# Kernel tuning notes

Hardware: AMD Instinct MI355X
Metric: run time of the kernel (lower is better)

Reference implementation:

```python
import jax, jax.numpy as jnp
import numpy as np

TOP_K = 4


def setup_inputs() -> dict:
    key = jax.random.key(0)
    ks = jax.random.split(key, 5)
    B, T, D = 2, 1024, 1024
    P, PD = 256, 32  # n_patterns, pattern_dim
    return {
        "x": jax.random.normal(ks[0], (B, T, D), dtype=jnp.float32),
        "hasher_w": jax.random.normal(ks[1], (PD, D), dtype=jnp.float32) * 0.03,
        "keys": jax.random.normal(ks[2], (P, PD), dtype=jnp.float32) * 0.1,
        "values_down": jax.random.normal(ks[3], (P, D, PD), dtype=jnp.float32) * 0.01,
        "values_up": jax.random.normal(ks[4], (P, PD, D), dtype=jnp.float32) * 0.01,
        "scale": jnp.full((1,), 0.1, dtype=jnp.float32),
    }


def reference(x, hasher_w, keys, values_down, values_up, scale):
    # h = hasher(x): [B,T,pattern_dim]
    h = jnp.einsum("btd,pd->btp", x, hasher_w)
    # similarity to pattern keys: [B,T,n_patterns]
    sim = jnp.einsum("btp,np->btn", h, keys)
    vals, idx = jax.lax.top_k(sim, TOP_K)          # [B,T,TOP_K]
    w = jax.nn.softmax(vals, axis=-1)              # softmax over the top-k scores
    out = jnp.zeros_like(x)
    for k in range(TOP_K):  # small fixed loop, matches original
        ik = idx[..., k]                            # [B,T] int32
        vd = values_down[ik]                        # [B,T,D,PD] gathered per-token
        vu = values_up[ik]                          # [B,T,PD,D]
        proj = jax.nn.silu(jnp.einsum("btd,btdp->btp", x, vd))
        o = jnp.einsum("btp,btpd->btd", proj, vu)
        out = out + o * w[..., k:k + 1]
    return x + out * scale
```

## Files before the change

### kernel.cpp

```cpp
#include <hip/hip_runtime.h>
#include <math.h>
#include <float.h>

#define DDIM 1024
#define PDIM 32
#define NPAT 256
#define TOPK 4
#define BLOCK 256
#define GT   16
#define DCHP 128
#define NCHP 8
#define RTPB 4

__global__ __launch_bounds__(BLOCK) void route_kernel(
    const float* __restrict__ x,
    const float* __restrict__ hasher_w,
    const float* __restrict__ keys,
    int*   __restrict__ tki,
    float* __restrict__ tkw,
    int*   __restrict__ gcount,
    int ntok)
{
    __shared__ float shmem[RTPB * 64 * 33];
    __shared__ float h_s[RTPB][32];

    const int tid  = threadIdx.x;
    const int wv   = tid >> 6;
    const int lane = tid & 63;
    const int traw = blockIdx.x * RTPB + wv;
    const int tok  = min(traw, ntok - 1);

    const float4* xrow = (const float4*)(x + (size_t)tok * DDIM);
    float4 xr[4];
    #pragma unroll
    for (int i = 0; i < 4; ++i) xr[i] = xrow[i * 64 + lane];

    float part[PDIM];
    #pragma unroll
    for (int pp = 0; pp < PDIM; ++pp) part[pp] = 0.f;

    float* hs = shmem;
    for (int i = 0; i < 4; ++i) {
        #pragma unroll
        for (int k = 0; k < 8; ++k) {
            const int q  = k * 256 + tid;
            const int pp = q >> 6, fi = q & 63;
            ((float4*)hs)[q] =
                *(const float4*)(hasher_w + (size_t)pp * DDIM + i * 256 + fi * 4);
        }
        __syncthreads();
        #pragma unroll
        for (int pp = 0; pp < PDIM; ++pp) {
            const float4 w4 = *(const float4*)&hs[pp * 256 + lane * 4];
            part[pp] = fmaf(xr[i].x, w4.x, part[pp]);
            part[pp] = fmaf(xr[i].y, w4.y, part[pp]);
            part[pp] = fmaf(xr[i].z, w4.z, part[pp]);
            part[pp] = fmaf(xr[i].w, w4.w, part[pp]);
        }
        __syncthreads();
    }

    float* P = shmem + wv * (64 * 33);
    #pragma unroll
    for (int pp = 0; pp < PDIM; ++pp) P[lane * 33 + pp] = part[pp];
    __syncthreads();

    {
        const int pp = lane & 31, half = lane >> 5;
        float hsum = 0.f;
        #pragma unroll 8
        for (int i = 0; i < 32; ++i)
            hsum += P[(half * 32 + i) * 33 + pp];
        hsum += __shfl_xor(hsum, 32, 64);
        if (half == 0) h_s[wv][pp] = hsum;
    }
    __syncthreads();

    float4 h4[8];
    #pragma unroll
    for (int i = 0; i < 8; ++i) h4[i] = *(const float4*)&h_s[wv][i * 4];

    float sc0, sc1, sc2, sc3;
    {
        float sv[4];
        #pragma unroll
        for (int c = 0; c < 4; ++c) {
            const float4* kr = (const float4*)(keys + (size_t)(c * 64 + lane) * PDIM);
            float a = 0.f;
            #pragma unroll
            for (int i = 0; i < 8; ++i) {
                const float4 k4 = kr[i];
                a = fmaf(k4.x, h4[i].x, a); a = fmaf(k4.y, h4[i].y, a);
                a = fmaf(k4.z, h4[i].z, a); a = fmaf(k4.w, h4[i].w, a);
            }
            sv[c] = a;
        }
        sc0 = sv[0]; sc1 = sv[1]; sc2 = sv[2]; sc3 = sv[3];
    }

    float wval[TOPK]; int widx[TOPK];
    #pragma unroll
    for (int r = 0; r < TOPK; ++r) {
        float bv = sc0; int bc = 0;
        if (sc1 > bv) { bv = sc1; bc = 1; }
        if (sc2 > bv) { bv = sc2; bc = 2; }
        if (sc3 > bv) { bv = sc3; bc = 3; }
        int bidx = bc * 64 + lane;
        #pragma unroll
        for (int off = 1; off < 64; off <<= 1) {
            const float ov = __shfl_xor(bv, off, 64);
            const int   oi = __shfl_xor(bidx, off, 64);
            if (ov > bv || (ov == bv && oi < bidx)) { bv = ov; bidx = oi; }
        }
        wval[r] = bv; widx[r] = bidx;
        if ((bidx & 63) == lane) {
            const int c = bidx >> 6;
            if (c == 0) sc0 = -FLT_MAX;
            else if (c == 1) sc1 = -FLT_MAX;
            else if (c == 2) sc2 = -FLT_MAX;
            else sc3 = -FLT_MAX;
        }
    }

    if (lane == 0 && traw < ntok) {
        float m = wval[0];
        #pragma unroll
        for (int k = 1; k < TOPK; ++k) m = fmaxf(m, wval[k]);
        float s = 0.f, e[TOPK];
        #pragma unroll
        for (int k = 0; k < TOPK; ++k) { e[k] = expf(wval[k] - m); s += e[k]; }
        #pragma unroll
        for (int k = 0; k < TOPK; ++k) {
            tki[tok * TOPK + k] = widx[k];
            tkw[tok * TOPK + k] = e[k] / s;
            atomicAdd(&gcount[widx[k]], 1);
        }
    }
}

__global__ __launch_bounds__(NPAT) void scan_kernel(
    const int* __restrict__ gcount,
    int* __restrict__ offs,
    int* __restrict__ gcur,
    int* __restrict__ tile2p, int* __restrict__ tilei,
    int maxt)
{
    __shared__ int s[NPAT];
    const int tid = threadIdx.x;

    const int v = gcount[tid];
    s[tid] = v;
    __syncthreads();
    for (int off = 1; off < NPAT; off <<= 1) {
        int t = 0;
        if (tid >= off) t = s[tid - off];
        __syncthreads();
        s[tid] += t;
        __syncthreads();
    }
    const int incl = s[tid];
    offs[tid + 1] = incl;
    if (tid == 0) offs[0] = 0;
    gcur[tid] = incl - v;

    const int tc = (v + GT - 1) / GT;
    __syncthreads();
    s[tid] = tc;
    __syncthreads();
    for (int off = 1; off < NPAT; off <<= 1) {
        int t = 0;
        if (tid >= off) t = s[tid - off];
        __syncthreads();
        s[tid] += t;
        __syncthreads();
    }
    const int toff = s[tid] - tc;
    for (int i = tid; i < maxt; i += NPAT) tile2p[i] = -1;
    __syncthreads();
    for (int i = 0; i < tc; ++i) { tile2p[toff + i] = tid; tilei[toff + i] = i; }
}

__global__ __launch_bounds__(BLOCK) void fill_kernel(
    const int* __restrict__ tki, const float* __restrict__ tkw,
    const float* __restrict__ scale_p,
    int* __restrict__ gcur,
    int* __restrict__ etok, float* __restrict__ ew, int* __restrict__ slotof,
    int nent)
{
    const int e = blockIdx.x * BLOCK + threadIdx.x;
    if (e >= nent) return;
    const int p = tki[e];
    const int slot = atomicAdd(&gcur[p], 1);
    etok[slot] = e >> 2;
    ew[slot]   = tkw[e] * scale_p[0];
    slotof[e]  = slot;
}

__global__ __launch_bounds__(BLOCK, 6) void proj_kernel(
    const float* __restrict__ x,
    const float* __restrict__ vd,
    const int* __restrict__ offs,
    const int* __restrict__ etok,
    const int* __restrict__ tile2p,
    const int* __restrict__ tilei,
    float* __restrict__ part,
    int nent)
{
    __shared__ float vd_s[DCHP * PDIM];
    __shared__ float x_s[GT * DCHP];
    __shared__ int   gt[GT];
    __shared__ int   gs[GT];

    const int tb  = blockIdx.x >> 3;
    const int c   = blockIdx.x & 7;
    const int p   = tile2p[tb];
    if (p < 0) return;
    const int tid = threadIdx.x;
    const int off0 = offs[p] + tilei[tb] * GT;
    const int gv   = min(GT, offs[p + 1] - off0);

    const float* vdp = vd + (size_t)p * DDIM * PDIM + (size_t)c * DCHP * PDIM;
    #pragma unroll
    for (int k = 0; k < 4; ++k)
        ((float4*)vd_s)[k * 256 + tid] = ((const float4*)vdp)[k * 256 + tid];

    if (tid < GT) {
        if (tid < gv) { gt[tid] = etok[off0 + tid]; gs[tid] = off0 + tid; }
        else          { gt[tid] = etok[off0];       gs[tid] = nent; }
    }
    __syncthreads();

    #pragma unroll
    for (int k = 0; k < 2; ++k) {
        const int q  = k * 256 + tid;
        const int g  = q >> 5, fi = q & 31;
        ((float4*)x_s)[g * 32 + fi] =
            *(const float4*)(x + (size_t)gt[g] * DDIM + c * DCHP + fi * 4);
    }
    __syncthreads();

    const int lane = tid & 63;
    const int wv   = tid >> 6;
    const int pp4  = lane & 7;
    const int seg  = lane >> 3;

    float4 acc[4];
    #pragma unroll
    for (int j = 0; j < 4; ++j) acc[j] = make_float4(0.f, 0.f, 0.f, 0.f);

    #pragma unroll
    for (int i4 = 0; i4 < 4; ++i4) {
        const int d0 = seg * 16 + i4 * 4;
        const float4 v0 = *(const float4*)&vd_s[(d0 + 0) * PDIM + pp4 * 4];
        const float4 v1 = *(const float4*)&vd_s[(d0 + 1) * PDIM + pp4 * 4];
        const float4 v2 = *(const float4*)&vd_s[(d0 + 2) * PDIM + pp4 * 4];
        const float4 v3 = *(const float4*)&vd_s[(d0 + 3) * PDIM + pp4 * 4];
        #pragma unroll
        for (int j = 0; j < 4; ++j) {
            const float4 xg = *(const float4*)&x_s[(wv * 4 + j) * DCHP + d0];
            acc[j].x = fmaf(xg.x, v0.x, acc[j].x);
            acc[j].y = fmaf(xg.x, v0.y, acc[j].y);
            acc[j].z = fmaf(xg.x, v0.z, acc[j].z);
            acc[j].w = fmaf(xg.x, v0.w, acc[j].w);
            acc[j].x = fmaf(xg.y, v1.x, acc[j].x);
            acc[j].y = fmaf(xg.y, v1.y, acc[j].y);
            acc[j].z = fmaf(xg.y, v1.z, acc[j].z);
            acc[j].w = fmaf(xg.y, v1.w, acc[j].w);
            acc[j].x = fmaf(xg.z, v2.x, acc[j].x);
            acc[j].y = fmaf(xg.z, v2.y, acc[j].y);
            acc[j].z = fmaf(xg.z, v2.z, acc[j].z);
            acc[j].w = fmaf(xg.z, v2.w, acc[j].w);
            acc[j].x = fmaf(xg.w, v3.x, acc[j].x);
            acc[j].y = fmaf(xg.w, v3.y, acc[j].y);
            acc[j].z = fmaf(xg.w, v3.z, acc[j].z);
            acc[j].w = fmaf(xg.w, v3.w, acc[j].w);
        }
    }

    #pragma unroll
    for (int j = 0; j < 4; ++j) {
        #pragma unroll
        for (int off = 8; off <= 32; off <<= 1) {
            acc[j].x += __shfl_xor(acc[j].x, off, 64);
            acc[j].y += __shfl_xor(acc[j].y, off, 64);
            acc[j].z += __shfl_xor(acc[j].z, off, 64);
            acc[j].w += __shfl_xor(acc[j].w, off, 64);
        }
    }

    float* partc = part + (size_t)c * (size_t)(nent + 1) * PDIM;
    if ((lane & 0x38) == 0) {
        #pragma unroll
        for (int j = 0; j < 4; ++j)
            *(float4*)&partc[(size_t)gs[wv * 4 + j] * PDIM + pp4 * 4] = acc[j];
    }
}

template <int MODE>
__global__ __launch_bounds__(BLOCK, 6) void up_kernel(
    const float* __restrict__ vu,
    const int* __restrict__ offs,
    const int* __restrict__ etok,
    const float* __restrict__ ew,
    const int* __restrict__ tile2p,
    const int* __restrict__ tilei,
    const float* __restrict__ part,
    float* __restrict__ dst,
    int nent)
{
    __shared__ float vu_s[PDIM * DCHP];
    __shared__ float projT[PDIM][20];
    __shared__ int   gt[GT];
    __shared__ float gw[GT];
    __shared__ int   gs[GT];

    const int tb  = blockIdx.x >> 3;
    const int c   = blockIdx.x & 7;
    const int p   = tile2p[tb];
    if (p < 0) return;
    const int tid = threadIdx.x;
    const int off0 = offs[p] + tilei[tb] * GT;
    const int gv   = min(GT, offs[p + 1] - off0);

    const size_t PS = (size_t)(nent + 1) * PDIM;

    const float* vup = vu + (size_t)p * PDIM * DDIM + (size_t)c * DCHP;
    #pragma unroll
    for (int k = 0; k < 4; ++k) {
        const int q  = k * 256 + tid;
        const int pp = q >> 5, fi = q & 31;
        *(float4*)&vu_s[pp * DCHP + fi * 4] =
            *(const float4*)(vup + (size_t)pp * DDIM + fi * 4);
    }
    if (tid < GT) {
        if (tid < gv) {
            gt[tid] = etok[off0 + tid];
            gw[tid] = ew[off0 + tid];
            gs[tid] = off0 + tid;
        } else {
            gt[tid] = etok[off0]; gw[tid] = 0.f; gs[tid] = nent;
        }
    }
    __syncthreads();

    #pragma unroll
    for (int r = 0; r < 2; ++r) {
        const int idx = tid + r * BLOCK;
        const int g = idx >> 5, pp = idx & 31;
        const size_t row = (size_t)gs[g] * PDIM + pp;
        float s = 0.f;
        #pragma unroll
        for (int i = 0; i < NCHP; ++i) s += part[i * PS + row];
        const float pj = s / (1.f + expf(-s));
        projT[pp][g] = pj * gw[g];
    }
    __syncthreads();

    const int tg  = tid >> 5;
    const int l32 = tid & 31;
    const int g0 = tg * 2, g1 = tg * 2 + 1;

    float4 o0 = make_float4(0.f, 0.f, 0.f, 0.f);
    float4 o1 = o0;
    #pragma unroll
    for (int pp = 0; pp < PDIM; ++pp) {
        const float4 vu4 = *(const float4*)&vu_s[pp * DCHP + l32 * 4];
        const float a = projT[pp][g0];
        const float b = projT[pp][g1];
        o0.x = fmaf(a, vu4.x, o0.x); o0.y = fmaf(a, vu4.y, o0.y);
        o0.z = fmaf(a, vu4.z, o0.z); o0.w = fmaf(a, vu4.w, o0.w);
        o1.x = fmaf(b, vu4.x, o1.x); o1.y = fmaf(b, vu4.y, o1.y);
        o1.z = fmaf(b, vu4.z, o1.z); o1.w = fmaf(b, vu4.w, o1.w);
    }

    if (MODE == 0) {
        *(float4*)(dst + (size_t)gs[g0] * DDIM + c * DCHP + l32 * 4) = o0;
        *(float4*)(dst + (size_t)gs[g1] * DDIM + c * DCHP + l32 * 4) = o1;
    } else {
        if (g0 < gv) {
            float* op = dst + (size_t)gt[g0] * DDIM + c * DCHP + l32 * 4;
            atomicAdd(op + 0, o0.x); atomicAdd(op + 1, o0.y);
            atomicAdd(op + 2, o0.z); atomicAdd(op + 3, o0.w);
        }
        if (g1 < gv) {
            float* op = dst + (size_t)gt[g1] * DDIM + c * DCHP + l32 * 4;
            atomicAdd(op + 0, o1.x); atomicAdd(op + 1, o1.y);
            atomicAdd(op + 2, o1.z); atomicAdd(op + 3, o1.w);
        }
    }
}

__global__ __launch_bounds__(BLOCK) void combine_kernel(
    const float* __restrict__ x, const float* __restrict__ contrib,
    const int* __restrict__ slotof, float* __restrict__ out)
{
    __shared__ int sl[TOPK];
    const int t = blockIdx.x, tid = threadIdx.x;
    if (tid < TOPK) sl[tid] = slotof[t * TOPK + tid];
    __syncthreads();
    float4 r = ((const float4*)(x + (size_t)t * DDIM))[tid];
    #pragma unroll
    for (int k = 0; k < TOPK; ++k) {
        const float4 cv = ((const float4*)(contrib + (size_t)sl[k] * DDIM))[tid];
        r.x += cv.x; r.y += cv.y; r.z += cv.z; r.w += cv.w;
    }
    ((float4*)(out + (size_t)t * DDIM))[tid] = r;
}

extern "C" void kernel_launch(void* const* d_in, const int* in_sizes, int n_in,
                              void* d_out, int out_size, void* d_ws, size_t ws_size,
                              hipStream_t stream) {
    const float* x        = (const float*)d_in[0];
    const float* hasher_w = (const float*)d_in[1];
    const float* keys     = (const float*)d_in[2];
    const float* vd       = (const float*)d_in[3];
    const float* vu       = (const float*)d_in[4];
    const float* scale    = (const float*)d_in[5];
    float* out = (float*)d_out;

    const int ntok = in_sizes[0] / DDIM;
    if (ntok <= 0) return;
    const int nent = ntok * TOPK;
    const int maxt = (nent + GT - 1) / GT + NPAT;

    char* w = (char*)d_ws;
    const size_t o_gcnt = 0;
    const size_t o_gcur = 1024;
    const size_t o_offs = 2048;
    const size_t o_tki  = 4096;
    const size_t o_tkw  = o_tki  + (size_t)nent * 4;
    const size_t o_etok = o_tkw  + (size_t)nent * 4;
    const size_t o_ew   = o_etok + (size_t)nent * 4;
    const size_t o_slot = o_ew   + (size_t)nent * 4;
    const size_t o_t2p  = o_slot + (size_t)nent * 4;
    const size_t o_tli  = o_t2p  + (size_t)maxt * 4;
    const size_t o_part = (o_tli + (size_t)maxt * 4 + 255) & ~(size_t)255;
    const size_t partsz = (size_t)NCHP * (size_t)(nent + 1) * PDIM * 4;
    const size_t o_ctb  = (o_part + partsz + 255) & ~(size_t)255;
    const size_t needPart    = o_ctb;
    const size_t needContrib = o_ctb + (size_t)(nent + 1) * DDIM * 4;

    int*   gcount = (int*)(w + o_gcnt);
    int*   gcur   = (int*)(w + o_gcur);
    int*   offs   = (int*)(w + o_offs);
    int*   tki    = (int*)(w + o_tki);
    float* tkw    = (float*)(w + o_tkw);
    int*   etok   = (int*)(w + o_etok);
    float* ew     = (float*)(w + o_ew);
    int*   slotof = (int*)(w + o_slot);
    int*   tile2p = (int*)(w + o_t2p);
    int*   tilei  = (int*)(w + o_tli);
    float* part   = (float*)(w + o_part);
    float* contrib= (float*)(w + o_ctb);

    hipMemsetAsync(gcount, 0, NPAT * sizeof(int), stream);

    const int rblocks = (ntok + RTPB - 1) / RTPB;
    hipLaunchKernelGGL(route_kernel, dim3(rblocks), dim3(BLOCK), 0, stream,
                       x, hasher_w, keys, tki, tkw, gcount, ntok);
    hipLaunchKernelGGL(scan_kernel, dim3(1), dim3(NPAT), 0, stream,
                       gcount, offs, gcur, tile2p, tilei, maxt);
    hipLaunchKernelGGL(fill_kernel, dim3((nent + BLOCK - 1) / BLOCK), dim3(BLOCK),
                       0, stream, tki, tkw, scale, gcur, etok, ew, slotof, nent);
    hipLaunchKernelGGL(proj_kernel, dim3(maxt * NCHP), dim3(BLOCK), 0, stream,
                       x, vd, offs, etok, tile2p, tilei, part, nent);

    if (ws_size >= needContrib) {
        hipLaunchKernelGGL((up_kernel<0>), dim3(maxt * NCHP), dim3(BLOCK), 0, stream,
                           vu, offs, etok, ew, tile2p, tilei, part, contrib, nent);
        hipLaunchKernelGGL(combine_kernel, dim3(ntok), dim3(BLOCK), 0, stream,
                           x, contrib, slotof, out);
    } else if (ws_size >= needPart) {
        hipMemcpyAsync(out, x, (size_t)ntok * DDIM * 4, hipMemcpyDeviceToDevice,
                       stream);
        hipLaunchKernelGGL((up_kernel<1>), dim3(maxt * NCHP), dim3(BLOCK), 0, stream,
                           vu, offs, etok, ew, tile2p, tilei, part, out, nent);
    }
}
```

Baseline: 186.0 us.

## Fuse down and up projections into one kernel, route two tokens per wave

The separate proj and up kernels are merged into one fused kernel per tile. It loops over all eight D-chunks, first for the down projection (accumulated in registers) and then for the up projection. This removes the partial-sum workspace round-trip and one launch. The catch is eight times fewer blocks, each running a serial chunk loop with many barriers, under launch bounds lowered to 3. The routing kernel now handles two tokens per wave, reusing each staged hasher tile for twice the FMAs.

```diff
diff --git a/kernel.cpp b/kernel.cpp
--- a/kernel.cpp
+++ b/kernel.cpp
@@ -10,7 +10,7 @@
 #define GT   16
 #define DCHP 128
 #define NCHP 8
-#define RTPB 4
+#define RTPB 8
 
 __global__ __launch_bounds__(BLOCK) void route_kernel(
     const float* __restrict__ x,
@@ -21,23 +21,28 @@
     int*   __restrict__ gcount,
     int ntok)
 {
-    __shared__ float shmem[RTPB * 64 * 33];
-    __shared__ float h_s[RTPB][32];
+    __shared__ float shmem[4 * 64 * 33];
+    __shared__ float h_s[4][2][PDIM];
 
     const int tid  = threadIdx.x;
     const int wv   = tid >> 6;
     const int lane = tid & 63;
-    const int traw = blockIdx.x * RTPB + wv;
-    const int tok  = min(traw, ntok - 1);
-
-    const float4* xrow = (const float4*)(x + (size_t)tok * DDIM);
-    float4 xr[4];
-    #pragma unroll
-    for (int i = 0; i < 4; ++i) xr[i] = xrow[i * 64 + lane];
-
-    float part[PDIM];
-    #pragma unroll
-    for (int pp = 0; pp < PDIM; ++pp) part[pp] = 0.f;
+    const int traw0 = blockIdx.x * RTPB + wv * 2;
+    const int traw1 = traw0 + 1;
+    const int tok0 = min(traw0, ntok - 1);
+    const int tok1 = min(traw1, ntok - 1);
+
+    float4 xr0[4], xr1[4];
+    {
+        const float4* p0 = (const float4*)(x + (size_t)tok0 * DDIM);
+        const float4* p1 = (const float4*)(x + (size_t)tok1 * DDIM);
+        #pragma unroll
+        for (int i = 0; i < 4; ++i) { xr0[i] = p0[i * 64 + lane]; xr1[i] = p1[i * 64 + lane]; }
+    }
+
+    float part0[PDIM], part1[PDIM];
+    #pragma unroll
+    for (int pp = 0; pp < PDIM; ++pp) { part0[pp] = 0.f; part1[pp] = 0.f; }
 
     float* hs = shmem;
     for (int i = 0; i < 4; ++i) {
@@ -52,88 +57,101 @@
         #pragma unroll
         for (int pp = 0; pp < PDIM; ++pp) {
             const float4 w4 = *(const float4*)&hs[pp * 256 + lane * 4];
-            part[pp] = fmaf(xr[i].x, w4.x, part[pp]);
-            part[pp] = fmaf(xr[i].y, w4.y, part[pp]);
-            part[pp] = fmaf(xr[i].z, w4.z, part[pp]);
-            part[pp] = fmaf(xr[i].w, w4.w, part[pp]);
+            part0[pp] = fmaf(xr0[i].x, w4.x, part0[pp]);
+            part0[pp] = fmaf(xr0[i].y, w4.y, part0[pp]);
+            part0[pp] = fmaf(xr0[i].z, w4.z, part0[pp]);
+            part0[pp] = fmaf(xr0[i].w, w4.w, part0[pp]);
+            part1[pp] = fmaf(xr1[i].x, w4.x, part1[pp]);
+            part1[pp] = fmaf(xr1[i].y, w4.y, part1[pp]);
+            part1[pp] = fmaf(xr1[i].z, w4.z, part1[pp]);
+            part1[pp] = fmaf(xr1[i].w, w4.w, part1[pp]);
         }
         __syncthreads();
     }
 
     float* P = shmem + wv * (64 * 33);
     #pragma unroll
-    for (int pp = 0; pp < PDIM; ++pp) P[lane * 33 + pp] = part[pp];
-    __syncthreads();
-
-    {
-        const int pp = lane & 31, half = lane >> 5;
-        float hsum = 0.f;
-        #pragma unroll 8
-        for (int i = 0; i < 32; ++i)
-            hsum += P[(half * 32 + i) * 33 + pp];
-        hsum += __shfl_xor(hsum, 32, 64);
-        if (half == 0) h_s[wv][pp] = hsum;
-    }
-    __syncthreads();
-
-    float4 h4[8];
-    #pragma unroll
-    for (int i = 0; i < 8; ++i) h4[i] = *(const float4*)&h_s[wv][i * 4];
-
-    float sc0, sc1, sc2, sc3;
-    {
-        float sv[4];
-        #pragma unroll
-        for (int c = 0; c < 4; ++c) {
-            const float4* kr = (const float4*)(keys + (size_t)(c * 64 + lane) * PDIM);
-            float a = 0.f;
-            #pragma unroll
-            for (int i = 0; i < 8; ++i) {
-                const float4 k4 = kr[i];
-                a = fmaf(k4.x, h4[i].x, a); a = fmaf(k4.y, h4[i].y, a);
-                a = fmaf(k4.z, h4[i].z, a); a = fmaf(k4.w, h4[i].w, a);
-            }
-            sv[c] = a;
-        }
-        sc0 = sv[0]; sc1 = sv[1]; sc2 = sv[2]; sc3 = sv[3];
-    }
-
-    float wval[TOPK]; int widx[TOPK];
-    #pragma unroll
-    for (int r = 0; r < TOPK; ++r) {
-        float bv = sc0; int bc = 0;
-        if (sc1 > bv) { bv = sc1; bc = 1; }
-        if (sc2 > bv) { bv = sc2; bc = 2; }
-        if (sc3 > bv) { bv = sc3; bc = 3; }
-        int bidx = bc * 64 + lane;
-        #pragma unroll
-        for (int off = 1; off < 64; off <<= 1) {
-            const float ov = __shfl_xor(bv, off, 64);
-            const int   oi = __shfl_xor(bidx, off, 64);
-            if (ov > bv || (ov == bv && oi < bidx)) { bv = ov; bidx = oi; }
-        }
-        wval[r] = bv; widx[r] = bidx;
-        if ((bidx & 63) == lane) {
-            const int c = bidx >> 6;
-            if (c == 0) sc0 = -FLT_MAX;
-            else if (c == 1) sc1 = -FLT_MAX;
-            else if (c == 2) sc2 = -FLT_MAX;
-            else sc3 = -FLT_MAX;
-        }
-    }
-
-    if (lane == 0 && traw < ntok) {
-        float m = wval[0];
-        #pragma unroll
-        for (int k = 1; k < TOPK; ++k) m = fmaxf(m, wval[k]);
-        float s = 0.f, e[TOPK];
-        #pragma unroll
-        for (int k = 0; k < TOPK; ++k) { e[k] = expf(wval[k] - m); s += e[k]; }
-        #pragma unroll
-        for (int k = 0; k < TOPK; ++k) {
-            tki[tok * TOPK + k] = widx[k];
-            tkw[tok * TOPK + k] = e[k] / s;
-            atomicAdd(&gcount[widx[k]], 1);
+    for (int t = 0; t < 2; ++t) {
+        const float* part = t ? part1 : part0;
+        #pragma unroll
+        for (int pp = 0; pp < PDIM; ++pp) P[lane * 33 + pp] = part[pp];
+        __syncthreads();
+        {
+            const int pp = lane & 31, half = lane >> 5;
+            float hsum = 0.f;
+            #pragma unroll 8
+            for (int i = 0; i < 32; ++i)
+                hsum += P[(half * 32 + i) * 33 + pp];
+            hsum += __shfl_xor(hsum, 32, 64);
+            if (half == 0) h_s[wv][t][pp] = hsum;
+        }
+        __syncthreads();
+    }
+
+    #pragma unroll
+    for (int t = 0; t < 2; ++t) {
+        const int traw = t ? traw1 : traw0;
+        const int tok  = t ? tok1  : tok0;
+
+        float4 h4[8];
+        #pragma unroll
+        for (int i = 0; i < 8; ++i) h4[i] = *(const float4*)&h_s[wv][t][i * 4];
+
+        float sc0, sc1, sc2, sc3;
+        {
+            float sv[4];
+            #pragma unroll
+            for (int c = 0; c < 4; ++c) {
+                const float4* kr = (const float4*)(keys + (size_t)(c * 64 + lane) * PDIM);
+                float a = 0.f;
+                #pragma unroll
+                for (int i = 0; i < 8; ++i) {
+                    const float4 k4 = kr[i];
+                    a = fmaf(k4.x, h4[i].x, a); a = fmaf(k4.y, h4[i].y, a);
+                    a = fmaf(k4.z, h4[i].z, a); a = fmaf(k4.w, h4[i].w, a);
+                }
+                sv[c] = a;
+            }
+            sc0 = sv[0]; sc1 = sv[1]; sc2 = sv[2]; sc3 = sv[3];
+        }
+
+        float wval[TOPK]; int widx[TOPK];
+        #pragma unroll
+        for (int r = 0; r < TOPK; ++r) {
+            float bv = sc0; int bc = 0;
+            if (sc1 > bv) { bv = sc1; bc = 1; }
+            if (sc2 > bv) { bv = sc2; bc = 2; }
+            if (sc3 > bv) { bv = sc3; bc = 3; }
+            int bidx = bc * 64 + lane;
+            #pragma unroll
+            for (int off = 1; off < 64; off <<= 1) {
+                const float ov = __shfl_xor(bv, off, 64);
+                const int   oi = __shfl_xor(bidx, off, 64);
+                if (ov > bv || (ov == bv && oi < bidx)) { bv = ov; bidx = oi; }
+            }
+            wval[r] = bv; widx[r] = bidx;
+            if ((bidx & 63) == lane) {
+                const int c = bidx >> 6;
+                if (c == 0) sc0 = -FLT_MAX;
+                else if (c == 1) sc1 = -FLT_MAX;
+                else if (c == 2) sc2 = -FLT_MAX;
+                else sc3 = -FLT_MAX;
+            }
+        }
+
+        if (lane == 0 && traw < ntok) {
+            float m = wval[0];
+            #pragma unroll
+            for (int k = 1; k < TOPK; ++k) m = fmaxf(m, wval[k]);
+            float s = 0.f, e[TOPK];
+            #pragma unroll
+            for (int k = 0; k < TOPK; ++k) { e[k] = expf(wval[k] - m); s += e[k]; }
+            #pragma unroll
+            for (int k = 0; k < TOPK; ++k) {
+                tki[tok * TOPK + k] = widx[k];
+                tkw[tok * TOPK + k] = e[k] / s;
+                atomicAdd(&gcount[widx[k]], 1);
+            }
         }
     }
 }
@@ -196,142 +214,33 @@
     slotof[e]  = slot;
 }
 
-__global__ __launch_bounds__(BLOCK, 6) void proj_kernel(
+template <int MODE>
+__global__ __launch_bounds__(BLOCK, 3) void fused_kernel(
     const float* __restrict__ x,
     const float* __restrict__ vd,
-    const int* __restrict__ offs,
-    const int* __restrict__ etok,
-    const int* __restrict__ tile2p,
-    const int* __restrict__ tilei,
-    float* __restrict__ part,
-    int nent)
-{
-    __shared__ float vd_s[DCHP * PDIM];
-    __shared__ float x_s[GT * DCHP];
-    __shared__ int   gt[GT];
-    __shared__ int   gs[GT];
-
-    const int tb  = blockIdx.x >> 3;
-    const int c   = blockIdx.x & 7;
-    const int p   = tile2p[tb];
-    if (p < 0) return;
-    const int tid = threadIdx.x;
-    const int off0 = offs[p] + tilei[tb] * GT;
-    const int gv   = min(GT, offs[p + 1] - off0);
-
-    const float* vdp = vd + (size_t)p * DDIM * PDIM + (size_t)c * DCHP * PDIM;
-    #pragma unroll
-    for (int k = 0; k < 4; ++k)
-        ((float4*)vd_s)[k * 256 + tid] = ((const float4*)vdp)[k * 256 + tid];
-
-    if (tid < GT) {
-        if (tid < gv) { gt[tid] = etok[off0 + tid]; gs[tid] = off0 + tid; }
-        else          { gt[tid] = etok[off0];       gs[tid] = nent; }
-    }
-    __syncthreads();
-
-    #pragma unroll
-    for (int k = 0; k < 2; ++k) {
-        const int q  = k * 256 + tid;
-        const int g  = q >> 5, fi = q & 31;
-        ((float4*)x_s)[g * 32 + fi] =
-            *(const float4*)(x + (size_t)gt[g] * DDIM + c * DCHP + fi * 4);
-    }
-    __syncthreads();
-
-    const int lane = tid & 63;
-    const int wv   = tid >> 6;
-    const int pp4  = lane & 7;
-    const int seg  = lane >> 3;
-
-    float4 acc[4];
-    #pragma unroll
-    for (int j = 0; j < 4; ++j) acc[j] = make_float4(0.f, 0.f, 0.f, 0.f);
-
-    #pragma unroll
-    for (int i4 = 0; i4 < 4; ++i4) {
-        const int d0 = seg * 16 + i4 * 4;
-        const float4 v0 = *(const float4*)&vd_s[(d0 + 0) * PDIM + pp4 * 4];
-        const float4 v1 = *(const float4*)&vd_s[(d0 + 1) * PDIM + pp4 * 4];
-        const float4 v2 = *(const float4*)&vd_s[(d0 + 2) * PDIM + pp4 * 4];
-        const float4 v3 = *(const float4*)&vd_s[(d0 + 3) * PDIM + pp4 * 4];
-        #pragma unroll
-        for (int j = 0; j < 4; ++j) {
-            const float4 xg = *(const float4*)&x_s[(wv * 4 + j) * DCHP + d0];
-            acc[j].x = fmaf(xg.x, v0.x, acc[j].x);
-            acc[j].y = fmaf(xg.x, v0.y, acc[j].y);
-            acc[j].z = fmaf(xg.x, v0.z, acc[j].z);
-            acc[j].w = fmaf(xg.x, v0.w, acc[j].w);
-            acc[j].x = fmaf(xg.y, v1.x, acc[j].x);
-            acc[j].y = fmaf(xg.y, v1.y, acc[j].y);
-            acc[j].z = fmaf(xg.y, v1.z, acc[j].z);
-            acc[j].w = fmaf(xg.y, v1.w, acc[j].w);
-            acc[j].x = fmaf(xg.z, v2.x, acc[j].x);
-            acc[j].y = fmaf(xg.z, v2.y, acc[j].y);
-            acc[j].z = fmaf(xg.z, v2.z, acc[j].z);
-            acc[j].w = fmaf(xg.z, v2.w, acc[j].w);
-            acc[j].x = fmaf(xg.w, v3.x, acc[j].x);
-            acc[j].y = fmaf(xg.w, v3.y, acc[j].y);
-            acc[j].z = fmaf(xg.w, v3.z, acc[j].z);
-            acc[j].w = fmaf(xg.w, v3.w, acc[j].w);
-        }
-    }
-
-    #pragma unroll
-    for (int j = 0; j < 4; ++j) {
-        #pragma unroll
-        for (int off = 8; off <= 32; off <<= 1) {
-            acc[j].x += __shfl_xor(acc[j].x, off, 64);
-            acc[j].y += __shfl_xor(acc[j].y, off, 64);
-            acc[j].z += __shfl_xor(acc[j].z, off, 64);
-            acc[j].w += __shfl_xor(acc[j].w, off, 64);
-        }
-    }
-
-    float* partc = part + (size_t)c * (size_t)(nent + 1) * PDIM;
-    if ((lane & 0x38) == 0) {
-        #pragma unroll
-        for (int j = 0; j < 4; ++j)
-            *(float4*)&partc[(size_t)gs[wv * 4 + j] * PDIM + pp4 * 4] = acc[j];
-    }
-}
-
-template <int MODE>
-__global__ __launch_bounds__(BLOCK, 6) void up_kernel(
     const float* __restrict__ vu,
     const int* __restrict__ offs,
     const int* __restrict__ etok,
     const float* __restrict__ ew,
     const int* __restrict__ tile2p,
     const int* __restrict__ tilei,
-    const float* __restrict__ part,
     float* __restrict__ dst,
     int nent)
 {
-    __shared__ float vu_s[PDIM * DCHP];
+    __shared__ float wbuf[DCHP * PDIM];
+    __shared__ float x_s[GT * DCHP];
     __shared__ float projT[PDIM][20];
     __shared__ int   gt[GT];
     __shared__ float gw[GT];
     __shared__ int   gs[GT];
 
-    const int tb  = blockIdx.x >> 3;
-    const int c   = blockIdx.x & 7;
-    const int p   = tile2p[tb];
+    const int tb = blockIdx.x;
+    const int p  = tile2p[tb];
     if (p < 0) return;
     const int tid = threadIdx.x;
     const int off0 = offs[p] + tilei[tb] * GT;
     const int gv   = min(GT, offs[p + 1] - off0);
 
-    const size_t PS = (size_t)(nent + 1) * PDIM;
-
-    const float* vup = vu + (size_t)p * PDIM * DDIM + (size_t)c * DCHP;
-    #pragma unroll
-    for (int k = 0; k < 4; ++k) {
-        const int q  = k * 256 + tid;
-        const int pp = q >> 5, fi = q & 31;
-        *(float4*)&vu_s[pp * DCHP + fi * 4] =
-            *(const float4*)(vup + (size_t)pp * DDIM + fi * 4);
-    }
     if (tid < GT) {
         if (tid < gv) {
             gt[tid] = etok[off0 + tid];
@@ -343,16 +252,82 @@
     }
     __syncthreads();
 
-    #pragma unroll
-    for (int r = 0; r < 2; ++r) {
-        const int idx = tid + r * BLOCK;
-        const int g = idx >> 5, pp = idx & 31;
-        const size_t row = (size_t)gs[g] * PDIM + pp;
-        float s = 0.f;
-        #pragma unroll
-        for (int i = 0; i < NCHP; ++i) s += part[i * PS + row];
-        const float pj = s / (1.f + expf(-s));
-        projT[pp][g] = pj * gw[g];
+    const int lane = tid & 63;
+    const int wv   = tid >> 6;
+    const int pp4  = lane & 7;
+    const int seg  = lane >> 3;
+
+    float4 acc[4];
+    #pragma unroll
+    for (int j = 0; j < 4; ++j) acc[j] = make_float4(0.f, 0.f, 0.f, 0.f);
+
+    const float* vdp = vd + (size_t)p * DDIM * PDIM;
+    for (int c = 0; c < NCHP; ++c) {
+        const float4* vsrc = (const float4*)(vdp + (size_t)c * DCHP * PDIM);
+        #pragma unroll
+        for (int k = 0; k < 4; ++k)
+            ((float4*)wbuf)[k * 256 + tid] = vsrc[k * 256 + tid];
+        #pragma unroll
+        for (int k = 0; k < 2; ++k) {
+            const int q  = k * 256 + tid;
+            const int g  = q >> 5, fi = q & 31;
+            ((float4*)x_s)[g * 32 + fi] =
+                *(const float4*)(x + (size_t)gt[g] * DDIM + c * DCHP + fi * 4);
+        }
+        __syncthreads();
+
+        #pragma unroll
+        for (int i4 = 0; i4 < 4; ++i4) {
+            const int d0 = seg * 16 + i4 * 4;
+            const float4 v0 = *(const float4*)&wbuf[(d0 + 0) * PDIM + pp4 * 4];
+            const float4 v1 = *(const float4*)&wbuf[(d0 + 1) * PDIM + pp4 * 4];
+            const float4 v2 = *(const float4*)&wbuf[(d0 + 2) * PDIM + pp4 * 4];
+            const float4 v3 = *(const float4*)&wbuf[(d0 + 3) * PDIM + pp4 * 4];
+            #pragma unroll
+            for (int j = 0; j < 4; ++j) {
+                const float4 xg = *(const float4*)&x_s[(wv * 4 + j) * DCHP + d0];
+                acc[j].x = fmaf(xg.x, v0.x, acc[j].x);
+                acc[j].y = fmaf(xg.x, v0.y, acc[j].y);
+                acc[j].z = fmaf(xg.x, v0.z, acc[j].z);
+                acc[j].w = fmaf(xg.x, v0.w, acc[j].w);
+                acc[j].x = fmaf(xg.y, v1.x, acc[j].x);
+                acc[j].y = fmaf(xg.y, v1.y, acc[j].y);
+                acc[j].z = fmaf(xg.y, v1.z, acc[j].z);
+                acc[j].w = fmaf(xg.y, v1.w, acc[j].w);
+                acc[j].x = fmaf(xg.z, v2.x, acc[j].x);
+                acc[j].y = fmaf(xg.z, v2.y, acc[j].y);
+                acc[j].z = fmaf(xg.z, v2.z, acc[j].z);
+                acc[j].w = fmaf(xg.z, v2.w, acc[j].w);
+                acc[j].x = fmaf(xg.w, v3.x, acc[j].x);
+                acc[j].y = fmaf(xg.w, v3.y, acc[j].y);
+                acc[j].z = fmaf(xg.w, v3.z, acc[j].z);
+                acc[j].w = fmaf(xg.w, v3.w, acc[j].w);
+            }
+        }
+        __syncthreads();
+    }
+
+    #pragma unroll
+    for (int j = 0; j < 4; ++j) {
+        #pragma unroll
+        for (int off = 8; off <= 32; off <<= 1) {
+            acc[j].x += __shfl_xor(acc[j].x, off, 64);
+            acc[j].y += __shfl_xor(acc[j].y, off, 64);
+            acc[j].z += __shfl_xor(acc[j].z, off, 64);
+            acc[j].w += __shfl_xor(acc[j].w, off, 64);
+        }
+    }
+    if ((lane & 0x38) == 0) {
+        #pragma unroll
+        for (int j = 0; j < 4; ++j) {
+            const int g = wv * 4 + j;
+            const float wgt = gw[g];
+            const float4 a = acc[j];
+            projT[pp4 * 4 + 0][g] = (a.x / (1.f + expf(-a.x))) * wgt;
+            projT[pp4 * 4 + 1][g] = (a.y / (1.f + expf(-a.y))) * wgt;
+            projT[pp4 * 4 + 2][g] = (a.z / (1.f + expf(-a.z))) * wgt;
+            projT[pp4 * 4 + 3][g] = (a.w / (1.f + expf(-a.w))) * wgt;
+        }
     }
     __syncthreads();
 
@@ -360,33 +335,46 @@
     const int l32 = tid & 31;
     const int g0 = tg * 2, g1 = tg * 2 + 1;
 
-    float4 o0 = make_float4(0.f, 0.f, 0.f, 0.f);
-    float4 o1 = o0;
-    #pragma unroll
-    for (int pp = 0; pp < PDIM; ++pp) {
-        const float4 vu4 = *(const float4*)&vu_s[pp * DCHP + l32 * 4];
-        const float a = projT[pp][g0];
-        const float b = projT[pp][g1];
-        o0.x = fmaf(a, vu4.x, o0.x); o0.y = fmaf(a, vu4.y, o0.y);
-        o0.z = fmaf(a, vu4.z, o0.z); o0.w = fmaf(a, vu4.w, o0.w);
-        o1.x = fmaf(b, vu4.x, o1.x); o1.y = fmaf(b, vu4.y, o1.y);
-        o1.z = fmaf(b, vu4.z, o1.z); o1.w = fmaf(b, vu4.w, o1.w);
-    }
-
-    if (MODE == 0) {
-        *(float4*)(dst + (size_t)gs[g0] * DDIM + c * DCHP + l32 * 4) = o0;
-        *(float4*)(dst + (size_t)gs[g1] * DDIM + c * DCHP + l32 * 4) = o1;
-    } else {
-        if (g0 < gv) {
-            float* op = dst + (size_t)gt[g0] * DDIM + c * DCHP + l32 * 4;
-            atomicAdd(op + 0, o0.x); atomicAdd(op + 1, o0.y);
-            atomicAdd(op + 2, o0.z); atomicAdd(op + 3, o0.w);
-        }
-        if (g1 < gv) {
-            float* op = dst + (size_t)gt[g1] * DDIM + c * DCHP + l32 * 4;
-            atomicAdd(op + 0, o1.x); atomicAdd(op + 1, o1.y);
-            atomicAdd(op + 2, o1.z); atomicAdd(op + 3, o1.w);
-        }
+    const float* vup = vu + (size_t)p * PDIM * DDIM;
+    for (int c = 0; c < NCHP; ++c) {
+        #pragma unroll
+        for (int k = 0; k < 4; ++k) {
+            const int q  = k * 256 + tid;
+            const int pp = q >> 5, fi = q & 31;
+            *(float4*)&wbuf[pp * DCHP + fi * 4] =
+                *(const float4*)(vup + (size_t)pp * DDIM + c * DCHP + fi * 4);
+        }
+        __syncthreads();
+
+        float4 o0 = make_float4(0.f, 0.f, 0.f, 0.f);
+        float4 o1 = o0;
+        #pragma unroll
+        for (int pp = 0; pp < PDIM; ++pp) {
+            const float4 vu4 = *(const float4*)&wbuf[pp * DCHP + l32 * 4];
+            const float a = projT[pp][g0];
+            const float b = projT[pp][g1];
+            o0.x = fmaf(a, vu4.x, o0.x); o0.y = fmaf(a, vu4.y, o0.y);
+            o0.z = fmaf(a, vu4.z, o0.z); o0.w = fmaf(a, vu4.w, o0.w);
+            o1.x = fmaf(b, vu4.x, o1.x); o1.y = fmaf(b, vu4.y, o1.y);
+            o1.z = fmaf(b, vu4.z, o1.z); o1.w = fmaf(b, vu4.w, o1.w);
+        }
+
+        if (MODE == 0) {
+            *(float4*)(dst + (size_t)gs[g0] * DDIM + c * DCHP + l32 * 4) = o0;
+            *(float4*)(dst + (size_t)gs[g1] * DDIM + c * DCHP + l32 * 4) = o1;
+        } else {
+            if (g0 < gv) {
+                float* op = dst + (size_t)gt[g0] * DDIM + c * DCHP + l32 * 4;
+                atomicAdd(op + 0, o0.x); atomicAdd(op + 1, o0.y);
+                atomicAdd(op + 2, o0.z); atomicAdd(op + 3, o0.w);
+            }
+            if (g1 < gv) {
+                float* op = dst + (size_t)gt[g1] * DDIM + c * DCHP + l32 * 4;
+                atomicAdd(op + 0, o1.x); atomicAdd(op + 1, o1.y);
+                atomicAdd(op + 2, o1.z); atomicAdd(op + 3, o1.w);
+            }
+        }
+        __syncthreads();
     }
 }
 
@@ -434,9 +422,7 @@
     const size_t o_slot = o_ew   + (size_t)nent * 4;
     const size_t o_t2p  = o_slot + (size_t)nent * 4;
     const size_t o_tli  = o_t2p  + (size_t)maxt * 4;
-    const size_t o_part = (o_tli + (size_t)maxt * 4 + 255) & ~(size_t)255;
-    const size_t partsz = (size_t)NCHP * (size_t)(nent + 1) * PDIM * 4;
-    const size_t o_ctb  = (o_part + partsz + 255) & ~(size_t)255;
+    const size_t o_ctb  = (o_tli + (size_t)maxt * 4 + 255) & ~(size_t)255;
     const size_t needPart    = o_ctb;
     const size_t needContrib = o_ctb + (size_t)(nent + 1) * DDIM * 4;
 
@@ -450,7 +436,6 @@
     int*   slotof = (int*)(w + o_slot);
     int*   tile2p = (int*)(w + o_t2p);
     int*   tilei  = (int*)(w + o_tli);
-    float* part   = (float*)(w + o_part);
     float* contrib= (float*)(w + o_ctb);
 
     hipMemsetAsync(gcount, 0, NPAT * sizeof(int), stream);
@@ -462,18 +447,16 @@
                        gcount, offs, gcur, tile2p, tilei, maxt);
     hipLaunchKernelGGL(fill_kernel, dim3((nent + BLOCK - 1) / BLOCK), dim3(BLOCK),
                        0, stream, tki, tkw, scale, gcur, etok, ew, slotof, nent);
-    hipLaunchKernelGGL(proj_kernel, dim3(maxt * NCHP), dim3(BLOCK), 0, stream,
-                       x, vd, offs, etok, tile2p, tilei, part, nent);
 
     if (ws_size >= needContrib) {
-        hipLaunchKernelGGL((up_kernel<0>), dim3(maxt * NCHP), dim3(BLOCK), 0, stream,
-                           vu, offs, etok, ew, tile2p, tilei, part, contrib, nent);
+        hipLaunchKernelGGL((fused_kernel<0>), dim3(maxt), dim3(BLOCK), 0, stream,
+                           x, vd, vu, offs, etok, ew, tile2p, tilei, contrib, nent);
         hipLaunchKernelGGL(combine_kernel, dim3(ntok), dim3(BLOCK), 0, stream,
                            x, contrib, slotof, out);
     } else if (ws_size >= needPart) {
         hipMemcpyAsync(out, x, (size_t)ntok * DDIM * 4, hipMemcpyDeviceToDevice,
                        stream);
-        hipLaunchKernelGGL((up_kernel<1>), dim3(maxt * NCHP), dim3(BLOCK), 0, stream,
-                           vu, offs, etok, ew, tile2p, tilei, part, out, nent);
-    }
-}
+        hipLaunchKernelGGL((fused_kernel<1>), dim3(maxt), dim3(BLOCK), 0, stream,
+                           x, vd, vu, offs, etok, ew, tile2p, tilei, out, nent);
+    }
+}
```

Measured after the change: 195.6 us. 5.2% more time.

## Loop over D chunks inside proj kernel and fuse SiLU and weighting

Applied to the files above, without the earlier changes.

Each proj block now processes half a token tile (8 entries) and iterates over all eight D chunks, double-buffering the values_down chunk in shared memory. It produces the final SiLU-activated, gate-weighted projection directly. This removes the eight-way partial-sum buffer and the reduction plus SiLU step in the up kernel, cutting global traffic and work there. The cost is fewer, longer proj blocks: x is read directly from global memory per wave, each block streams the full 128KB of values_down for its pattern, and occupancy drops to 4 blocks per CU.

```diff
diff --git a/kernel.cpp b/kernel.cpp
--- a/kernel.cpp
+++ b/kernel.cpp
@@ -8,6 +8,7 @@
 #define TOPK 4
 #define BLOCK 256
 #define GT   16
+#define HT   8
 #define DCHP 128
 #define NCHP 8
 #define RTPB 4
@@ -196,18 +197,148 @@
     slotof[e]  = slot;
 }
 
-__global__ __launch_bounds__(BLOCK, 6) void proj_kernel(
+__global__ __launch_bounds__(BLOCK, 4) void proj_kernel(
     const float* __restrict__ x,
     const float* __restrict__ vd,
     const int* __restrict__ offs,
     const int* __restrict__ etok,
+    const float* __restrict__ ew,
     const int* __restrict__ tile2p,
     const int* __restrict__ tilei,
-    float* __restrict__ part,
+    float* __restrict__ projW,
     int nent)
 {
-    __shared__ float vd_s[DCHP * PDIM];
-    __shared__ float x_s[GT * DCHP];
+    __shared__ float vd_s[2][DCHP * PDIM];
+    __shared__ int   gt[HT];
+    __shared__ float gw[HT];
+    __shared__ int   gs[HT];
+
+    const int tb = blockIdx.x >> 1;
+    const int hf = blockIdx.x & 1;
+    const int p  = tile2p[tb];
+    if (p < 0) return;
+    const int tid  = threadIdx.x;
+    const int off0 = offs[p] + tilei[tb] * GT + hf * HT;
+    const int gv   = min(HT, offs[p + 1] - off0);
+    if (gv <= 0) return;
+
+    if (tid < HT) {
+        if (tid < gv) { gt[tid] = etok[off0 + tid]; gw[tid] = ew[off0 + tid]; gs[tid] = off0 + tid; }
+        else          { gt[tid] = etok[off0];       gw[tid] = 0.f;            gs[tid] = nent; }
+    }
+
+    const float* vdp = vd + (size_t)p * DDIM * PDIM;
+
+    {
+        const float4* vsrc = (const float4*)vdp;
+        #pragma unroll
+        for (int k = 0; k < 4; ++k)
+            ((float4*)vd_s[0])[k * 256 + tid] = vsrc[k * 256 + tid];
+    }
+    __syncthreads();
+
+    const int lane = tid & 63;
+    const int wv   = tid >> 6;
+    const int pp4  = lane & 7;
+    const int seg  = lane >> 3;
+    const int g0 = wv * 2, g1 = wv * 2 + 1;
+    const float* xb0 = x + (size_t)gt[g0] * DDIM;
+    const float* xb1 = x + (size_t)gt[g1] * DDIM;
+
+    float4 acc0 = make_float4(0.f, 0.f, 0.f, 0.f);
+    float4 acc1 = acc0;
+
+    for (int c = 0; c < NCHP; ++c) {
+        const int cur = c & 1;
+        float4 st0, st1, st2, st3;
+        if (c < NCHP - 1) {
+            const float4* vsrc = (const float4*)(vdp + (size_t)(c + 1) * DCHP * PDIM);
+            st0 = vsrc[0 * 256 + tid];
+            st1 = vsrc[1 * 256 + tid];
+            st2 = vsrc[2 * 256 + tid];
+            st3 = vsrc[3 * 256 + tid];
+        }
+
+        #pragma unroll
+        for (int i4 = 0; i4 < 4; ++i4) {
+            const int d0 = seg * 16 + i4 * 4;
+            const float* vb = &vd_s[cur][d0 * PDIM + pp4 * 4];
+            const float4 v0 = *(const float4*)(vb + 0 * PDIM);
+            const float4 v1 = *(const float4*)(vb + 1 * PDIM);
+            const float4 v2 = *(const float4*)(vb + 2 * PDIM);
+            const float4 v3 = *(const float4*)(vb + 3 * PDIM);
+            const float4 xg0 = *(const float4*)(xb0 + c * DCHP + d0);
+            const float4 xg1 = *(const float4*)(xb1 + c * DCHP + d0);
+
+            acc0.x = fmaf(xg0.x, v0.x, acc0.x); acc0.y = fmaf(xg0.x, v0.y, acc0.y);
+            acc0.z = fmaf(xg0.x, v0.z, acc0.z); acc0.w = fmaf(xg0.x, v0.w, acc0.w);
+            acc0.x = fmaf(xg0.y, v1.x, acc0.x); acc0.y = fmaf(xg0.y, v1.y, acc0.y);
+            acc0.z = fmaf(xg0.y, v1.z, acc0.z); acc0.w = fmaf(xg0.y, v1.w, acc0.w);
+            acc0.x = fmaf(xg0.z, v2.x, acc0.x); acc0.y = fmaf(xg0.z, v2.y, acc0.y);
+            acc0.z = fmaf(xg0.z, v2.z, acc0.z); acc0.w = fmaf(xg0.z, v2.w, acc0.w);
+            acc0.x = fmaf(xg0.w, v3.x, acc0.x); acc0.y = fmaf(xg0.w, v3.y, acc0.y);
+            acc0.z = fmaf(xg0.w, v3.z, acc0.z); acc0.w = fmaf(xg0.w, v3.w, acc0.w);
+
+            acc1.x = fmaf(xg1.x, v0.x, acc1.x); acc1.y = fmaf(xg1.x, v0.y, acc1.y);
+            acc1.z = fmaf(xg1.x, v0.z, acc1.z); acc1.w = fmaf(xg1.x, v0.w, acc1.w);
+            acc1.x = fmaf(xg1.y, v1.x, acc1.x); acc1.y = fmaf(xg1.y, v1.y, acc1.y);
+            acc1.z = fmaf(xg1.y, v1.z, acc1.z); acc1.w = fmaf(xg1.y, v1.w, acc1.w);
+            acc1.x = fmaf(xg1.z, v2.x, acc1.x); acc1.y = fmaf(xg1.z, v2.y, acc1.y);
+            acc1.z = fmaf(xg1.z, v2.z, acc1.z); acc1.w = fmaf(xg1.z, v2.w, acc1.w);
+            acc1.x = fmaf(xg1.w, v3.x, acc1.x); acc1.y = fmaf(xg1.w, v3.y, acc1.y);
+            acc1.z = fmaf(xg1.w, v3.z, acc1.z); acc1.w = fmaf(xg1.w, v3.w, acc1.w);
+        }
+
+        if (c < NCHP - 1) {
+            const int nxt = cur ^ 1;
+            ((float4*)vd_s[nxt])[0 * 256 + tid] = st0;
+            ((float4*)vd_s[nxt])[1 * 256 + tid] = st1;
+            ((float4*)vd_s[nxt])[2 * 256 + tid] = st2;
+            ((float4*)vd_s[nxt])[3 * 256 + tid] = st3;
+            __syncthreads();
+        }
+    }
+
+    #pragma unroll
+    for (int off = 8; off <= 32; off <<= 1) {
+        acc0.x += __shfl_xor(acc0.x, off, 64);
+        acc0.y += __shfl_xor(acc0.y, off, 64);
+        acc0.z += __shfl_xor(acc0.z, off, 64);
+        acc0.w += __shfl_xor(acc0.w, off, 64);
+        acc1.x += __shfl_xor(acc1.x, off, 64);
+        acc1.y += __shfl_xor(acc1.y, off, 64);
+        acc1.z += __shfl_xor(acc1.z, off, 64);
+        acc1.w += __shfl_xor(acc1.w, off, 64);
+    }
+    if ((lane & 0x38) == 0) {
+        const float w0 = gw[g0], w1 = gw[g1];
+        float4 o0, o1;
+        o0.x = (acc0.x / (1.f + expf(-acc0.x))) * w0;
+        o0.y = (acc0.y / (1.f + expf(-acc0.y))) * w0;
+        o0.z = (acc0.z / (1.f + expf(-acc0.z))) * w0;
+        o0.w = (acc0.w / (1.f + expf(-acc0.w))) * w0;
+        o1.x = (acc1.x / (1.f + expf(-acc1.x))) * w1;
+        o1.y = (acc1.y / (1.f + expf(-acc1.y))) * w1;
+        o1.z = (acc1.z / (1.f + expf(-acc1.z))) * w1;
+        o1.w = (acc1.w / (1.f + expf(-acc1.w))) * w1;
+        *(float4*)&projW[(size_t)gs[g0] * PDIM + pp4 * 4] = o0;
+        *(float4*)&projW[(size_t)gs[g1] * PDIM + pp4 * 4] = o1;
+    }
+}
+
+template <int MODE>
+__global__ __launch_bounds__(BLOCK, 6) void up_kernel(
+    const float* __restrict__ vu,
+    const int* __restrict__ offs,
+    const int* __restrict__ etok,
+    const int* __restrict__ tile2p,
+    const int* __restrict__ tilei,
+    const float* __restrict__ projW,
+    float* __restrict__ dst,
+    int nent)
+{
+    __shared__ float vu_s[PDIM * DCHP];
+    __shared__ float projT[PDIM][20];
     __shared__ int   gt[GT];
     __shared__ int   gs[GT];
 
@@ -219,111 +350,6 @@
     const int off0 = offs[p] + tilei[tb] * GT;
     const int gv   = min(GT, offs[p + 1] - off0);
 
-    const float* vdp = vd + (size_t)p * DDIM * PDIM + (size_t)c * DCHP * PDIM;
-    #pragma unroll
-    for (int k = 0; k < 4; ++k)
-        ((float4*)vd_s)[k * 256 + tid] = ((const float4*)vdp)[k * 256 + tid];
-
-    if (tid < GT) {
-        if (tid < gv) { gt[tid] = etok[off0 + tid]; gs[tid] = off0 + tid; }
-        else          { gt[tid] = etok[off0];       gs[tid] = nent; }
-    }
-    __syncthreads();
-
-    #pragma unroll
-    for (int k = 0; k < 2; ++k) {
-        const int q  = k * 256 + tid;
-        const int g  = q >> 5, fi = q & 31;
-        ((float4*)x_s)[g * 32 + fi] =
-            *(const float4*)(x + (size_t)gt[g] * DDIM + c * DCHP + fi * 4);
-    }
-    __syncthreads();
-
-    const int lane = tid & 63;
-    const int wv   = tid >> 6;
-    const int pp4  = lane & 7;
-    const int seg  = lane >> 3;
-
-    float4 acc[4];
-    #pragma unroll
-    for (int j = 0; j < 4; ++j) acc[j] = make_float4(0.f, 0.f, 0.f, 0.f);
-
-    #pragma unroll
-    for (int i4 = 0; i4 < 4; ++i4) {
-        const int d0 = seg * 16 + i4 * 4;
-        const float4 v0 = *(const float4*)&vd_s[(d0 + 0) * PDIM + pp4 * 4];
-        const float4 v1 = *(const float4*)&vd_s[(d0 + 1) * PDIM + pp4 * 4];
-        const float4 v2 = *(const float4*)&vd_s[(d0 + 2) * PDIM + pp4 * 4];
-        const float4 v3 = *(const float4*)&vd_s[(d0 + 3) * PDIM + pp4 * 4];
-        #pragma unroll
-        for (int j = 0; j < 4; ++j) {
-            const float4 xg = *(const float4*)&x_s[(wv * 4 + j) * DCHP + d0];
-            acc[j].x = fmaf(xg.x, v0.x, acc[j].x);
-            acc[j].y = fmaf(xg.x, v0.y, acc[j].y);
-            acc[j].z = fmaf(xg.x, v0.z, acc[j].z);
-            acc[j].w = fmaf(xg.x, v0.w, acc[j].w);
-            acc[j].x = fmaf(xg.y, v1.x, acc[j].x);
-            acc[j].y = fmaf(xg.y, v1.y, acc[j].y);
-            acc[j].z = fmaf(xg.y, v1.z, acc[j].z);
-            acc[j].w = fmaf(xg.y, v1.w, acc[j].w);
-            acc[j].x = fmaf(xg.z, v2.x, acc[j].x);
-            acc[j].y = fmaf(xg.z, v2.y, acc[j].y);
-            acc[j].z = fmaf(xg.z, v2.z, acc[j].z);
-            acc[j].w = fmaf(xg.z, v2.w, acc[j].w);
-            acc[j].x = fmaf(xg.w, v3.x, acc[j].x);
-            acc[j].y = fmaf(xg.w, v3.y, acc[j].y);
-            acc[j].z = fmaf(xg.w, v3.z, acc[j].z);
-            acc[j].w = fmaf(xg.w, v3.w, acc[j].w);
-        }
-    }
-
-    #pragma unroll
-    for (int j = 0; j < 4; ++j) {
-        #pragma unroll
-        for (int off = 8; off <= 32; off <<= 1) {
-            acc[j].x += __shfl_xor(acc[j].x, off, 64);
-            acc[j].y += __shfl_xor(acc[j].y, off, 64);
-            acc[j].z += __shfl_xor(acc[j].z, off, 64);
-            acc[j].w += __shfl_xor(acc[j].w, off, 64);
-        }
-    }
-
-    float* partc = part + (size_t)c * (size_t)(nent + 1) * PDIM;
-    if ((lane & 0x38) == 0) {
-        #pragma unroll
-        for (int j = 0; j < 4; ++j)
-            *(float4*)&partc[(size_t)gs[wv * 4 + j] * PDIM + pp4 * 4] = acc[j];
-    }
-}
-
-template <int MODE>
-__global__ __launch_bounds__(BLOCK, 6) void up_kernel(
-    const float* __restrict__ vu,
-    const int* __restrict__ offs,
-    const int* __restrict__ etok,
-    const float* __restrict__ ew,
-    const int* __restrict__ tile2p,
-    const int* __restrict__ tilei,
-    const float* __restrict__ part,
-    float* __restrict__ dst,
-    int nent)
-{
-    __shared__ float vu_s[PDIM * DCHP];
-    __shared__ float projT[PDIM][20];
-    __shared__ int   gt[GT];
-    __shared__ float gw[GT];
-    __shared__ int   gs[GT];
-
-    const int tb  = blockIdx.x >> 3;
-    const int c   = blockIdx.x & 7;
-    const int p   = tile2p[tb];
-    if (p < 0) return;
-    const int tid = threadIdx.x;
-    const int off0 = offs[p] + tilei[tb] * GT;
-    const int gv   = min(GT, offs[p + 1] - off0);
-
-    const size_t PS = (size_t)(nent + 1) * PDIM;
-
     const float* vup = vu + (size_t)p * PDIM * DDIM + (size_t)c * DCHP;
     #pragma unroll
     for (int k = 0; k < 4; ++k) {
@@ -333,13 +359,8 @@
             *(const float4*)(vup + (size_t)pp * DDIM + fi * 4);
     }
     if (tid < GT) {
-        if (tid < gv) {
-            gt[tid] = etok[off0 + tid];
-            gw[tid] = ew[off0 + tid];
-            gs[tid] = off0 + tid;
-        } else {
-            gt[tid] = etok[off0]; gw[tid] = 0.f; gs[tid] = nent;
-        }
+        if (tid < gv) { gt[tid] = etok[off0 + tid]; gs[tid] = off0 + tid; }
+        else          { gt[tid] = etok[off0];       gs[tid] = nent; }
     }
     __syncthreads();
 
@@ -347,12 +368,7 @@
     for (int r = 0; r < 2; ++r) {
         const int idx = tid + r * BLOCK;
         const int g = idx >> 5, pp = idx & 31;
-        const size_t row = (size_t)gs[g] * PDIM + pp;
-        float s = 0.f;
-        #pragma unroll
-        for (int i = 0; i < NCHP; ++i) s += part[i * PS + row];
-        const float pj = s / (1.f + expf(-s));
-        projT[pp][g] = pj * gw[g];
+        projT[pp][g] = projW[(size_t)gs[g] * PDIM + pp];
     }
     __syncthreads();
 
@@ -434,10 +450,10 @@
     const size_t o_slot = o_ew   + (size_t)nent * 4;
     const size_t o_t2p  = o_slot + (size_t)nent * 4;
     const size_t o_tli  = o_t2p  + (size_t)maxt * 4;
-    const size_t o_part = (o_tli + (size_t)maxt * 4 + 255) & ~(size_t)255;
-    const size_t partsz = (size_t)NCHP * (size_t)(nent + 1) * PDIM * 4;
-    const size_t o_ctb  = (o_part + partsz + 255) & ~(size_t)255;
-    const size_t needPart    = o_ctb;
+    const size_t o_pw   = (o_tli + (size_t)maxt * 4 + 255) & ~(size_t)255;
+    const size_t pwsz   = (size_t)(nent + 1) * PDIM * 4;
+    const size_t o_ctb  = (o_pw + pwsz + 255) & ~(size_t)255;
+    const size_t needPW      = o_ctb;
     const size_t needContrib = o_ctb + (size_t)(nent + 1) * DDIM * 4;
 
     int*   gcount = (int*)(w + o_gcnt);
@@ -450,7 +466,7 @@
     int*   slotof = (int*)(w + o_slot);
     int*   tile2p = (int*)(w + o_t2p);
     int*   tilei  = (int*)(w + o_tli);
-    float* part   = (float*)(w + o_part);
+    float* projW  = (float*)(w + o_pw);
     float* contrib= (float*)(w + o_ctb);
 
     hipMemsetAsync(gcount, 0, NPAT * sizeof(int), stream);
@@ -462,18 +478,18 @@
                        gcount, offs, gcur, tile2p, tilei, maxt);
     hipLaunchKernelGGL(fill_kernel, dim3((nent + BLOCK - 1) / BLOCK), dim3(BLOCK),
                        0, stream, tki, tkw, scale, gcur, etok, ew, slotof, nent);
-    hipLaunchKernelGGL(proj_kernel, dim3(maxt * NCHP), dim3(BLOCK), 0, stream,
-                       x, vd, offs, etok, tile2p, tilei, part, nent);
+    hipLaunchKernelGGL(proj_kernel, dim3(maxt * 2), dim3(BLOCK), 0, stream,
+                       x, vd, offs, etok, ew, tile2p, tilei, projW, nent);
 
     if (ws_size >= needContrib) {
-        hipLaunchKernelGGL((up_kernel<0>), dim3(maxt * NCHP), dim3(BLOCK), 0, stream,
-                           vu, offs, etok, ew, tile2p, tilei, part, contrib, nent);
+        hipLaunchKernelGGL((up_kernel<0>), dim3(maxt * 8), dim3(BLOCK), 0, stream,
+                           vu, offs, etok, tile2p, tilei, projW, contrib, nent);
         hipLaunchKernelGGL(combine_kernel, dim3(ntok), dim3(BLOCK), 0, stream,
                            x, contrib, slotof, out);
-    } else if (ws_size >= needPart) {
+    } else if (ws_size >= needPW) {
         hipMemcpyAsync(out, x, (size_t)ntok * DDIM * 4, hipMemcpyDeviceToDevice,
                        stream);
-        hipLaunchKernelGGL((up_kernel<1>), dim3(maxt * NCHP), dim3(BLOCK), 0, stream,
-                           vu, offs, etok, ew, tile2p, tilei, part, out, nent);
-    }
-}
+        hipLaunchKernelGGL((up_kernel<1>), dim3(maxt * 8), dim3(BLOCK), 0, stream,
+                           vu, offs, etok, tile2p, tilei, projW, out, nent);
+    }
+}
```

After: 197.5 us. +6.2%, slower.
